# Performance work log

Measured on AMD Instinct MI355X. Metric: run time of the kernel, lower is better.

The kernel has to match this reference:

```python
import jax, jax.numpy as jnp
import numpy as np

B, T, D, H = 32, 512, 512, 8
DH = D // H  # 64


def _pos_enc(t, d):
    # pos / 10000^(2i/d) for ALL i, then sin on even cols, cos on odd cols, scaled by sqrt(d)
    pos = np.arange(t, dtype=np.float64)[:, None]
    i = np.arange(d, dtype=np.float64)[None, :]
    ang = pos / np.power(10000.0, 2.0 * i / d)
    pe = np.empty((t, d), dtype=np.float64)
    pe[:, 0::2] = np.sin(ang[:, 0::2])
    pe[:, 1::2] = np.cos(ang[:, 1::2])
    return jnp.asarray(pe * np.sqrt(float(d)), dtype=jnp.float32)


def setup_inputs() -> dict:
    key = jax.random.key(0)
    ks = jax.random.split(key, 9)
    return {
        "queries": jax.random.normal(ks[0], (B, T, D), dtype=jnp.float32),
        "keys": jax.random.normal(ks[1], (B, T, D), dtype=jnp.float32),
        "query_masks": jax.random.randint(ks[2], (B,), 0, T, dtype=jnp.int32),
        "key_masks": jax.random.randint(ks[3], (B,), 0, T, dtype=jnp.int32),
        "W_Q": jax.random.normal(ks[4], (D, D), dtype=jnp.float32) * 0.05,
        "W_K": jax.random.normal(ks[5], (D, D), dtype=jnp.float32) * 0.05,
        "W_V": jax.random.normal(ks[6], (D, D), dtype=jnp.float32) * 0.05,
        "fw1": jax.random.normal(ks[7], (D, 4 * D), dtype=jnp.float32) * 0.05,
        "fw2": jax.random.normal(ks[8], (4 * D, D), dtype=jnp.float32) * 0.05,
    }


def reference(queries, keys, query_masks, key_masks, W_Q, W_K, W_V, fw1, fw2):
    pe = _pos_enc(T, D)  # [T, D]
    # Source bug kept: queries = posenc(queries); keys = posenc(queries)  -> keys input unused
    q1 = queries + pe[None]          # [B,T,D]
    k1 = q1 + pe[None]               # pos-encoded twice
    Q = q1 @ W_Q                     # [B,T,D]
    Kp = k1 @ W_K                    # [B,T,D]
    V = Kp @ W_V                     # source bug kept: values from projected keys
    # split heads (head-major fold in the original concat(split) idiom)
    Qh = Q.reshape(B, T, H, DH).transpose(2, 0, 1, 3)   # [H,B,T,dh]
    Kh = Kp.reshape(B, T, H, DH).transpose(2, 0, 1, 3)
    Vh = V.reshape(B, T, H, DH).transpose(2, 0, 1, 3)
    scores = jnp.einsum('hbqd,hbkd->hbqk', Qh, Kh) / jnp.sqrt(jnp.float32(DH))
    # source subtracts max over the QUERY axis (axis=1 of [H*B,T,T]) = axis 2 here
    scores = scores - scores.max(axis=2, keepdims=True)
    attn = jax.nn.softmax(scores, axis=-1)
    qmask = (jnp.arange(T)[None, :] < query_masks[:, None]).astype(jnp.float32)  # [B,T]
    attn = attn * qmask[None, :, :, None]
    out = jnp.einsum('hbqk,hbkd->hbqd', attn, Vh)       # [H,B,T,dh]
    result = out.transpose(1, 2, 0, 3).reshape(B, T, D) + q1  # residual with pos-encoded queries
    hidden = jax.nn.relu(result @ fw1)                  # [B,T,4D]
    result = result + hidden @ fw2                      # residual; no layer norm (use_layer_norm=False)
    return result
```

## Files before the change

kernel.cpp:

```cpp
#include <hip/hip_runtime.h>
#include <cstdint>
#include <cstddef>

typedef __bf16 bf16x8 __attribute__((ext_vector_type(8)));
typedef float f32x4 __attribute__((ext_vector_type(4)));
using u16 = unsigned short;
using u32 = unsigned int;

__device__ __forceinline__ u16 f2b(float f) {
  u32 u = __float_as_uint(f);
  u32 r = u + 0x7FFFu + ((u >> 16) & 1u);
  return (u16)(r >> 16);
}
__device__ __forceinline__ float b2f(u16 h) { return __uint_as_float((u32)h << 16); }

__device__ __forceinline__ void gload16(const void* g, void* l) {
  __builtin_amdgcn_global_load_lds((const __attribute__((address_space(1))) void*)g,
                                   (__attribute__((address_space(3))) void*)l, 16, 0, 0);
}

__device__ __forceinline__ u32 mapf(float f) {
  u32 u = __float_as_uint(f);
  return (u & 0x80000000u) ? ~u : (u | 0x80000000u);
}
__device__ __forceinline__ float unmapf(u32 k) {
  u32 u = (k & 0x80000000u) ? (k ^ 0x80000000u) : ~k;
  return __uint_as_float(u);
}
__device__ __forceinline__ u32 cvtpk(float lo, float hi) {
  u32 r;
  asm("v_cvt_pk_bf16_f32 %0, %1, %2" : "=v"(r) : "v"(lo), "v"(hi));
  return r;
}

#define MFMA __builtin_amdgcn_mfma_f32_16x16x32_bf16

__global__ void pe_kernel(float* __restrict__ pe) {
  int i = blockIdx.x * 256 + threadIdx.x;
  if (i >= 512 * 512) return;
  int t = i >> 9, d = i & 511;
  double ang = (double)t * exp((double)d * (-2.0 / 512.0) * log(10000.0));
  double v = (d & 1) ? cos(ang) : sin(ang);
  pe[i] = (float)(v * 22.627416997969522);
}

__global__ void wconv_kernel(const float* __restrict__ WQ, const float* __restrict__ WK,
                             const float* __restrict__ WV, const float* __restrict__ f1,
                             const float* __restrict__ f2,
                             u16* __restrict__ WQth, u16* __restrict__ WQtl,
                             u16* __restrict__ WKth, u16* __restrict__ WKtl,
                             u16* __restrict__ WKb, u16* __restrict__ WVt,
                             u16* __restrict__ f1t, u16* __restrict__ f2t) {
  int i = blockIdx.x * 256 + threadIdx.x;
  if (i < 262144) {
    int n = i >> 9, k = i & 511;
    float wq = WQ[k * 512 + n];
    u16 h = f2b(wq);
    WQth[i] = h;
    WQtl[i] = f2b(wq - b2f(h));
    float wk = WK[k * 512 + n];
    h = f2b(wk);
    WKth[i] = h;
    WKtl[i] = f2b(wk - b2f(h));
    WKb[i] = f2b(WK[i]);
    WVt[i] = f2b(WV[k * 512 + n]);
  } else if (i < 262144 + 1048576) {
    int i2 = i - 262144;
    int n = i2 >> 9, k = i2 & 511;
    f1t[i2] = f2b(f1[k * 2048 + n]);
  } else if (i < 262144 + 2097152) {
    int i3 = i - 262144 - 1048576;
    int n = i3 >> 11, k = i3 & 2047;
    f2t[i3] = f2b(f2[k * 512 + n]);
  }
}

__global__ void prep_kernel(const float* __restrict__ q, const float* __restrict__ pe,
                            u16* __restrict__ q1h, u16* __restrict__ q1l,
                            u16* __restrict__ k1h, u16* __restrict__ k1l,
                            u32* __restrict__ m0) {
  int i = blockIdx.x * 256 + threadIdx.x;
  if (i < 131072) m0[i] = 0u;
  if (i >= 32 * 512 * 512) return;
  int td = i & (262144 - 1);
  float p = pe[td];
  float q1 = q[i] + p;
  float k1 = q1 + p;
  u16 h = f2b(q1);
  q1h[i] = h;
  q1l[i] = f2b(q1 - b2f(h));
  h = f2b(k1);
  k1h[i] = h;
  k1l[i] = f2b(k1 - b2f(h));
}

#define GM_BF16 0
#define GM_RELU 2
#define GM_ADDF32 3

template <int MODE>
__global__ __launch_bounds__(256, 3) void gemm_bt(const u16* __restrict__ A,
                                                  const u16* __restrict__ B, int M, int N, int K,
                                                  u16* __restrict__ outb, float* __restrict__ outf,
                                                  const float* __restrict__ res) {
  __shared__ u16 As[128 * 32];
  __shared__ u16 Bs[128 * 32];
  const int tid = threadIdx.x, lane = tid & 63, w = tid >> 6;
  const int wm = w >> 1, wn = w & 1;
  const long aBase = (long)blockIdx.x * 128;
  const long bBase = (long)blockIdx.y * 128;
  f32x4 acc[4][4] = {};
  const int nk = K >> 5;
  for (int kt = 0; kt < nk; ++kt) {
#pragma unroll
    for (int i = 0; i < 2; ++i) {
      const int c = w * 2 + i;
      const int off = c * 1024 + lane * 16;
      const int r = off >> 6, cb = off & 63;
      gload16((const char*)A + ((aBase + r) * (long)K + (long)kt * 32) * 2 + cb,
              (char*)As + c * 1024);
      gload16((const char*)B + ((bBase + r) * (long)K + (long)kt * 32) * 2 + cb,
              (char*)Bs + c * 1024);
    }
    __syncthreads();
    bf16x8 af[4], bfr[4];
#pragma unroll
    for (int x = 0; x < 4; ++x) {
      af[x] = *(const bf16x8*)&As[(wm * 64 + x * 16 + (lane & 15)) * 32 + (lane >> 4) * 8];
      bfr[x] = *(const bf16x8*)&Bs[(wn * 64 + x * 16 + (lane & 15)) * 32 + (lane >> 4) * 8];
    }
#pragma unroll
    for (int mf = 0; mf < 4; ++mf)
#pragma unroll
      for (int nf = 0; nf < 4; ++nf)
        acc[mf][nf] = MFMA(af[mf], bfr[nf], acc[mf][nf], 0, 0, 0);
    __syncthreads();
  }
#pragma unroll
  for (int mf = 0; mf < 4; ++mf)
#pragma unroll
    for (int nf = 0; nf < 4; ++nf) {
      const long row0 = aBase + wm * 64 + mf * 16 + (lane >> 4) * 4;
      const long col = bBase + wn * 64 + nf * 16 + (lane & 15);
#pragma unroll
      for (int j = 0; j < 4; ++j) {
        float v = acc[mf][nf][j];
        const long row = row0 + j;
        if constexpr (MODE == GM_BF16)
          outb[row * N + col] = f2b(v);
        else if constexpr (MODE == GM_RELU)
          outb[row * N + col] = f2b(v > 0.f ? v : 0.f);
        else
          outf[row * N + col] = res[row * N + col] + v;
      }
    }
}

__global__ __launch_bounds__(256, 2) void gemm_split(const u16* __restrict__ Ah,
                                                     const u16* __restrict__ Al,
                                                     const u16* __restrict__ Bh,
                                                     const u16* __restrict__ Bl, int M, int N,
                                                     int K, u16* __restrict__ Oh,
                                                     u16* __restrict__ Ol) {
  __shared__ u16 Ash[4096], Asl[4096], Bsh[4096], Bsl[4096];
  const int tid = threadIdx.x, lane = tid & 63, w = tid >> 6;
  const int wm = w >> 1, wn = w & 1;
  const long aBase = (long)blockIdx.x * 128;
  const long bBase = (long)blockIdx.y * 128;
  f32x4 acc[4][4] = {};
  const int nk = K >> 5;
  for (int kt = 0; kt < nk; ++kt) {
#pragma unroll
    for (int i = 0; i < 2; ++i) {
      const int c = w * 2 + i;
      const int off = c * 1024 + lane * 16;
      const int r = off >> 6, cb = off & 63;
      long ga = ((aBase + r) * (long)K + (long)kt * 32) * 2 + cb;
      long gb = ((bBase + r) * (long)K + (long)kt * 32) * 2 + cb;
      gload16((const char*)Ah + ga, (char*)Ash + c * 1024);
      gload16((const char*)Al + ga, (char*)Asl + c * 1024);
      gload16((const char*)Bh + gb, (char*)Bsh + c * 1024);
      gload16((const char*)Bl + gb, (char*)Bsl + c * 1024);
    }
    __syncthreads();
    bf16x8 ah[4], al[4], bh[4], bl[4];
#pragma unroll
    for (int x = 0; x < 4; ++x) {
      int ao = (wm * 64 + x * 16 + (lane & 15)) * 32 + (lane >> 4) * 8;
      int bo = (wn * 64 + x * 16 + (lane & 15)) * 32 + (lane >> 4) * 8;
      ah[x] = *(const bf16x8*)&Ash[ao];
      al[x] = *(const bf16x8*)&Asl[ao];
      bh[x] = *(const bf16x8*)&Bsh[bo];
      bl[x] = *(const bf16x8*)&Bsl[bo];
    }
#pragma unroll
    for (int mf = 0; mf < 4; ++mf)
#pragma unroll
      for (int nf = 0; nf < 4; ++nf) {
        acc[mf][nf] = MFMA(ah[mf], bh[nf], acc[mf][nf], 0, 0, 0);
        acc[mf][nf] = MFMA(ah[mf], bl[nf], acc[mf][nf], 0, 0, 0);
        acc[mf][nf] = MFMA(al[mf], bh[nf], acc[mf][nf], 0, 0, 0);
      }
    __syncthreads();
  }
#pragma unroll
  for (int mf = 0; mf < 4; ++mf)
#pragma unroll
    for (int nf = 0; nf < 4; ++nf) {
      const long row0 = aBase + wm * 64 + mf * 16 + (lane >> 4) * 4;
      const long col = bBase + wn * 64 + nf * 16 + (lane & 15);
#pragma unroll
      for (int j = 0; j < 4; ++j) {
        float v = acc[mf][nf][j];
        const long row = row0 + j;
        u16 h = f2b(v);
        Oh[row * N + col] = h;
        Ol[row * N + col] = f2b(v - b2f(h));
      }
    }
}

__global__ __launch_bounds__(256, 4) void attn_colmax(const u16* __restrict__ Qh,
                                                      const u16* __restrict__ Ql,
                                                      const u16* __restrict__ Kh,
                                                      const u16* __restrict__ Kl,
                                                      u32* __restrict__ mg) {
  __shared__ u16 Qsh[4096], Qsl[4096];
  __shared__ u16 Ksh[4096], Ksl[4096];
  __shared__ u32 mloc[512];
  const int tid = threadIdx.x, lane = tid & 63, w = tid >> 6;
  const int ql = lane & 15, g = lane >> 4;
  const int hb = blockIdx.x, b = hb >> 3, h = hb & 7, qc = blockIdx.y;
  mloc[tid] = 0u;
  mloc[tid + 256] = 0u;
  const int srccb = 16 * ((lane & 7) ^ ((lane >> 3) & 7));
#pragma unroll
  for (int i = 0; i < 2; ++i) {
    const int c = w * 2 + i;
    const int r = c * 8 + (lane >> 3);
    long gb = ((long)(b * 512 + qc * 64 + r) * 512 + h * 64) * 2 + srccb;
    gload16((const char*)Qh + gb, (char*)Qsh + c * 1024);
    gload16((const char*)Ql + gb, (char*)Qsl + c * 1024);
  }
  __syncthreads();
  const int qrow = w * 16 + ql;
  const int sw0 = ((g * 16) ^ ((ql & 7) * 16)) >> 1;
  const int sw1 = ((64 + g * 16) ^ ((ql & 7) * 16)) >> 1;
  bf16x8 qh0 = *(const bf16x8*)&Qsh[qrow * 64 + sw0];
  bf16x8 ql0 = *(const bf16x8*)&Qsl[qrow * 64 + sw0];
  bf16x8 qh1 = *(const bf16x8*)&Qsh[qrow * 64 + sw1];
  bf16x8 ql1 = *(const bf16x8*)&Qsl[qrow * 64 + sw1];
  for (int kc = 0; kc < 8; ++kc) {
#pragma unroll
    for (int i = 0; i < 2; ++i) {
      const int c = w * 2 + i;
      const int r = c * 8 + (lane >> 3);
      long gb = ((long)(b * 512 + kc * 64 + r) * 512 + h * 64) * 2 + srccb;
      gload16((const char*)Kh + gb, (char*)Ksh + c * 1024);
      gload16((const char*)Kl + gb, (char*)Ksl + c * 1024);
    }
    __syncthreads();
#pragma unroll
    for (int kt = 0; kt < 4; ++kt) {
      const int krow = kt * 16 + ql;
      bf16x8 kh0 = *(const bf16x8*)&Ksh[krow * 64 + sw0];
      bf16x8 kl0 = *(const bf16x8*)&Ksl[krow * 64 + sw0];
      bf16x8 kh1 = *(const bf16x8*)&Ksh[krow * 64 + sw1];
      bf16x8 kl1 = *(const bf16x8*)&Ksl[krow * 64 + sw1];
      f32x4 acc = {0.f, 0.f, 0.f, 0.f};
      acc = MFMA(qh0, kh0, acc, 0, 0, 0);
      acc = MFMA(qh0, kl0, acc, 0, 0, 0);
      acc = MFMA(ql0, kh0, acc, 0, 0, 0);
      acc = MFMA(qh1, kh1, acc, 0, 0, 0);
      acc = MFMA(qh1, kl1, acc, 0, 0, 0);
      acc = MFMA(ql1, kh1, acc, 0, 0, 0);
      float v = fmaxf(fmaxf(acc[0], acc[1]), fmaxf(acc[2], acc[3]));
      v = fmaxf(v, __shfl_xor(v, 16));
      v = fmaxf(v, __shfl_xor(v, 32));
      if (lane < 16) atomicMax(&mloc[kc * 64 + kt * 16 + ql], mapf(v));
    }
    __syncthreads();
  }
  for (int k = tid; k < 512; k += 256) atomicMax(&mg[(long)hb * 512 + k], mloc[k]);
}

__global__ __launch_bounds__(256, 3) void attn_main(
    const u16* __restrict__ Qh, const u16* __restrict__ Ql, const u16* __restrict__ Kh,
    const u16* __restrict__ Kl, const u16* __restrict__ Vt, const u32* __restrict__ mg,
    const int* __restrict__ qmask, const u16* __restrict__ q1h, const u16* __restrict__ q1l,
    float* __restrict__ resf, u16* __restrict__ resb) {
  __shared__ u16 Qsh[4096], Qsl[4096];
  __shared__ u16 Ksh[4096], Ksl[4096];
  __shared__ float mks[512];
  const int tid = threadIdx.x, lane = tid & 63, w = tid >> 6;
  const int qll = lane & 15, g = lane >> 4;
  const int hb = blockIdx.x, b = hb >> 3, h = hb & 7, qc = blockIdx.y;
  const int qm = qmask[b];
  for (int k = tid; k < 512; k += 256) mks[k] = 0.125f * unmapf(mg[(long)hb * 512 + k]);
  const int srccb = 16 * ((lane & 7) ^ ((lane >> 3) & 7));
#pragma unroll
  for (int i = 0; i < 2; ++i) {
    const int c = w * 2 + i;
    const int r = c * 8 + (lane >> 3);
    long gb = ((long)(b * 512 + qc * 64 + r) * 512 + h * 64) * 2 + srccb;
    gload16((const char*)Qh + gb, (char*)Qsh + c * 1024);
    gload16((const char*)Ql + gb, (char*)Qsl + c * 1024);
  }
  __syncthreads();
  const int qrow = w * 16 + qll;
  const int sw0 = ((g * 16) ^ ((qll & 7) * 16)) >> 1;
  const int sw1 = ((64 + g * 16) ^ ((qll & 7) * 16)) >> 1;
  bf16x8 qh0 = *(const bf16x8*)&Qsh[qrow * 64 + sw0];
  bf16x8 qh1 = *(const bf16x8*)&Qsh[qrow * 64 + sw1];
  bf16x8 qlo0 = *(const bf16x8*)&Qsl[qrow * 64 + sw0];
  bf16x8 qlo1 = *(const bf16x8*)&Qsl[qrow * 64 + sw1];
  f32x4 o[4] = {};
  float mr = -3.0e38f, rsum = 0.f;
  const u16* vb = Vt + (long)(h * 64) * 16384 + b * 512;
  const int src0 = (g & 1) * 32 + qll;
  const int src1 = src0 + 16;
  const bool lowh = g < 2;
  for (int kc = 0; kc < 8; ++kc) {
    bf16x8 vf[2][4];
#pragma unroll
    for (int k2 = 0; k2 < 2; ++k2)
#pragma unroll
      for (int nf = 0; nf < 4; ++nf)
        vf[k2][nf] =
            *(const bf16x8*)&vb[(long)(nf * 16 + qll) * 16384 + (kc * 2 + k2) * 32 + g * 8];
#pragma unroll
    for (int i = 0; i < 2; ++i) {
      const int c = w * 2 + i;
      const int r = c * 8 + (lane >> 3);
      long gb = ((long)(b * 512 + kc * 64 + r) * 512 + h * 64) * 2 + srccb;
      gload16((const char*)Kh + gb, (char*)Ksh + c * 1024);
      gload16((const char*)Kl + gb, (char*)Ksl + c * 1024);
    }
    __syncthreads();
    f32x4 s4[4] = {};
#pragma unroll
    for (int kt = 0; kt < 4; ++kt) {
      const int krow = kt * 16 + qll;
      bf16x8 kh0 = *(const bf16x8*)&Ksh[krow * 64 + sw0];
      bf16x8 kl0 = *(const bf16x8*)&Ksl[krow * 64 + sw0];
      bf16x8 kh1 = *(const bf16x8*)&Ksh[krow * 64 + sw1];
      bf16x8 kl1 = *(const bf16x8*)&Ksl[krow * 64 + sw1];
      s4[kt] = MFMA(kh0, qh0, s4[kt], 0, 0, 0);
      s4[kt] = MFMA(kh0, qlo0, s4[kt], 0, 0, 0);
      s4[kt] = MFMA(kl0, qh0, s4[kt], 0, 0, 0);
      s4[kt] = MFMA(kh1, qh1, s4[kt], 0, 0, 0);
      s4[kt] = MFMA(kh1, qlo1, s4[kt], 0, 0, 0);
      s4[kt] = MFMA(kl1, qh1, s4[kt], 0, 0, 0);
    }
    __syncthreads();
    float pm = mr;
#pragma unroll
    for (int kt = 0; kt < 4; ++kt) {
      f32x4 mrow = *(const f32x4*)&mks[kc * 64 + kt * 16 + g * 4];
#pragma unroll
      for (int j = 0; j < 4; ++j) {
        float z = s4[kt][j] * 0.125f - mrow[j];
        s4[kt][j] = z;
        pm = fmaxf(pm, z);
      }
    }
    pm = fmaxf(pm, __shfl_xor(pm, 16));
    pm = fmaxf(pm, __shfl_xor(pm, 32));
    const float f = __expf(mr - pm);
    mr = pm;
    rsum *= f;
#pragma unroll
    for (int nf = 0; nf < 4; ++nf) {
      o[nf][0] *= f;
      o[nf][1] *= f;
      o[nf][2] *= f;
      o[nf][3] *= f;
    }
    u32 pk0[4], pk1[4];
#pragma unroll
    for (int kt = 0; kt < 4; ++kt) {
      float p0 = __expf(s4[kt][0] - mr);
      float p1 = __expf(s4[kt][1] - mr);
      float p2 = __expf(s4[kt][2] - mr);
      float p3 = __expf(s4[kt][3] - mr);
      rsum += (p0 + p1) + (p2 + p3);
      pk0[kt] = cvtpk(p0, p1);
      pk1[kt] = cvtpk(p2, p3);
    }
#pragma unroll
    for (int k2 = 0; k2 < 2; ++k2) {
      const int fA = 2 * k2, fB = 2 * k2 + 1;
      u32 a00 = __shfl(pk0[fA], src0), b00 = __shfl(pk0[fB], src0);
      u32 a10 = __shfl(pk1[fA], src0), b10 = __shfl(pk1[fB], src0);
      u32 a01 = __shfl(pk0[fA], src1), b01 = __shfl(pk0[fB], src1);
      u32 a11 = __shfl(pk1[fA], src1), b11 = __shfl(pk1[fB], src1);
      union {
        u32 u[4];
        bf16x8 v;
      } pf;
      pf.u[0] = lowh ? a00 : b00;
      pf.u[1] = lowh ? a10 : b10;
      pf.u[2] = lowh ? a01 : b01;
      pf.u[3] = lowh ? a11 : b11;
#pragma unroll
      for (int nf = 0; nf < 4; ++nf) o[nf] = MFMA(vf[k2][nf], pf.v, o[nf], 0, 0, 0);
    }
  }
  rsum += __shfl_xor(rsum, 16);
  rsum += __shfl_xor(rsum, 32);
  const int qg = qc * 64 + w * 16 + qll;
  const float sc = (qg < qm) ? (1.0f / rsum) : 0.0f;
#pragma unroll
  for (int nf = 0; nf < 4; ++nf) {
    const int col = h * 64 + nf * 16 + g * 4;
    const long idx = (long)(b * 512 + qg) * 512 + col;
    ushort4 qh4 = *(const ushort4*)&q1h[idx];
    ushort4 ql4 = *(const ushort4*)&q1l[idx];
    float v0 = o[nf][0] * sc + b2f(qh4.x) + b2f(ql4.x);
    float v1 = o[nf][1] * sc + b2f(qh4.y) + b2f(ql4.y);
    float v2 = o[nf][2] * sc + b2f(qh4.z) + b2f(ql4.z);
    float v3 = o[nf][3] * sc + b2f(qh4.w) + b2f(ql4.w);
    *(float4*)&resf[idx] = make_float4(v0, v1, v2, v3);
    ushort4 rb = {f2b(v0), f2b(v1), f2b(v2), f2b(v3)};
    *(ushort4*)&resb[idx] = rb;
  }
}

extern "C" void kernel_launch(void* const* d_in, const int* in_sizes, int n_in, void* d_out,
                              int out_size, void* d_ws, size_t ws_size, hipStream_t stream) {
  (void)in_sizes;
  (void)n_in;
  (void)out_size;
  (void)ws_size;
  const float* queries = (const float*)d_in[0];
  const int* qmask = (const int*)d_in[2];
  const float* WQ = (const float*)d_in[4];
  const float* WK = (const float*)d_in[5];
  const float* WV = (const float*)d_in[6];
  const float* f1 = (const float*)d_in[7];
  const float* f2 = (const float*)d_in[8];
  float* out = (float*)d_out;
  char* ws = (char*)d_ws;
  const size_t A = 16777216;
  u16* q1h = (u16*)(ws + 0 * A);
  u16* q1l = (u16*)(ws + 1 * A);
  u16* k1h = (u16*)(ws + 2 * A);
  u16* k1l = (u16*)(ws + 3 * A);
  u16* Qh = (u16*)(ws + 4 * A);
  u16* Ql = (u16*)(ws + 5 * A);
  u16* Kh = (u16*)(ws + 6 * A);
  u16* Kl = (u16*)(ws + 7 * A);
  u16* Vt = (u16*)(ws + 8 * A);
  u16* resb = (u16*)(ws + 9 * A);
  u16* hid = (u16*)(ws + 2 * A);
  hid = (u16*)(ws + 0 * A);
  float* pe = (float*)(ws + 10 * A);
  u32* m_ws = (u32*)(ws + 10 * A + 1048576);
  char* wbase = ws + 10 * A + 1572864;
  u16* WQth = (u16*)(wbase + 0 * 524288);
  u16* WQtl = (u16*)(wbase + 1 * 524288);
  u16* WKth = (u16*)(wbase + 2 * 524288);
  u16* WKtl = (u16*)(wbase + 3 * 524288);
  u16* WKb = (u16*)(wbase + 4 * 524288);
  u16* WVt_w = (u16*)(wbase + 5 * 524288);
  u16* WKVt = (u16*)(wbase + 6 * 524288);
  u16* f1t = (u16*)(wbase + 7 * 524288);
  u16* f2t = (u16*)(wbase + 7 * 524288 + 2097152);

  pe_kernel<<<1024, 256, 0, stream>>>(pe);
  wconv_kernel<<<9216, 256, 0, stream>>>(WQ, WK, WV, f1, f2, WQth, WQtl, WKth, WKtl, WKb, WVt_w,
                                         f1t, f2t);
  prep_kernel<<<32768, 256, 0, stream>>>(queries, pe, q1h, q1l, k1h, k1l, m_ws);
  gemm_bt<GM_BF16><<<dim3(4, 4), 256, 0, stream>>>(WVt_w, WKb, 512, 512, 512, WKVt, nullptr,
                                                   nullptr);
  gemm_split<<<dim3(128, 4), 256, 0, stream>>>(q1h, q1l, WQth, WQtl, 16384, 512, 512, Qh, Ql);
  gemm_split<<<dim3(128, 4), 256, 0, stream>>>(k1h, k1l, WKth, WKtl, 16384, 512, 512, Kh, Kl);
  gemm_bt<GM_BF16><<<dim3(4, 128), 256, 0, stream>>>(WKVt, k1h, 512, 16384, 512, Vt, nullptr,
                                                     nullptr);
  attn_colmax<<<dim3(256, 8), 256, 0, stream>>>(Qh, Ql, Kh, Kl, m_ws);
  attn_main<<<dim3(256, 8), 256, 0, stream>>>(Qh, Ql, Kh, Kl, Vt, m_ws, qmask, q1h, q1l, out,
                                              resb);
  gemm_bt<GM_RELU><<<dim3(128, 16), 256, 0, stream>>>(resb, f1t, 16384, 2048, 512, hid, nullptr,
                                                      nullptr);
  gemm_bt<GM_ADDF32><<<dim3(128, 4), 256, 0, stream>>>(hid, f2t, 16384, 512, 2048, nullptr, out,
                                                       out);
}
```

Baseline: 365.0 us.

## Load Q/K fragments directly from global memory in attention kernels, dropping LDS staging

Both attention kernels (the column-max pass and the main pass) now read Q and K MFMA fragments straight from global memory into registers instead of staging them through swizzled shared memory, which removes the LDS buffers and most of the block barriers. The column-max kernel also drops its shared-memory max reduction and issues atomicMax directly to global memory. This cuts LDS use and synchronization, which may raise occupancy, but K tiles are now fetched redundantly by each of the four waves through cache and there are many more global atomics.

```diff
diff --git a/kernel.cpp b/kernel.cpp
--- a/kernel.cpp
+++ b/kernel.cpp
@@ -225,48 +225,23 @@
                                                       const u16* __restrict__ Kh,
                                                       const u16* __restrict__ Kl,
                                                       u32* __restrict__ mg) {
-  __shared__ u16 Qsh[4096], Qsl[4096];
-  __shared__ u16 Ksh[4096], Ksl[4096];
-  __shared__ u32 mloc[512];
   const int tid = threadIdx.x, lane = tid & 63, w = tid >> 6;
-  const int ql = lane & 15, g = lane >> 4;
+  const int qll = lane & 15, g = lane >> 4;
   const int hb = blockIdx.x, b = hb >> 3, h = hb & 7, qc = blockIdx.y;
-  mloc[tid] = 0u;
-  mloc[tid + 256] = 0u;
-  const int srccb = 16 * ((lane & 7) ^ ((lane >> 3) & 7));
-#pragma unroll
-  for (int i = 0; i < 2; ++i) {
-    const int c = w * 2 + i;
-    const int r = c * 8 + (lane >> 3);
-    long gb = ((long)(b * 512 + qc * 64 + r) * 512 + h * 64) * 2 + srccb;
-    gload16((const char*)Qh + gb, (char*)Qsh + c * 1024);
-    gload16((const char*)Ql + gb, (char*)Qsl + c * 1024);
-  }
-  __syncthreads();
-  const int qrow = w * 16 + ql;
-  const int sw0 = ((g * 16) ^ ((ql & 7) * 16)) >> 1;
-  const int sw1 = ((64 + g * 16) ^ ((ql & 7) * 16)) >> 1;
-  bf16x8 qh0 = *(const bf16x8*)&Qsh[qrow * 64 + sw0];
-  bf16x8 ql0 = *(const bf16x8*)&Qsl[qrow * 64 + sw0];
-  bf16x8 qh1 = *(const bf16x8*)&Qsh[qrow * 64 + sw1];
-  bf16x8 ql1 = *(const bf16x8*)&Qsl[qrow * 64 + sw1];
+  const long qrow = (long)(b * 512 + qc * 64 + w * 16 + qll) * 512 + h * 64 + g * 8;
+  bf16x8 qh0 = *(const bf16x8*)&Qh[qrow];
+  bf16x8 qh1 = *(const bf16x8*)&Qh[qrow + 32];
+  bf16x8 ql0 = *(const bf16x8*)&Ql[qrow];
+  bf16x8 ql1 = *(const bf16x8*)&Ql[qrow + 32];
+  u32* mghb = mg + (long)hb * 512;
   for (int kc = 0; kc < 8; ++kc) {
 #pragma unroll
-    for (int i = 0; i < 2; ++i) {
-      const int c = w * 2 + i;
-      const int r = c * 8 + (lane >> 3);
-      long gb = ((long)(b * 512 + kc * 64 + r) * 512 + h * 64) * 2 + srccb;
-      gload16((const char*)Kh + gb, (char*)Ksh + c * 1024);
-      gload16((const char*)Kl + gb, (char*)Ksl + c * 1024);
-    }
-    __syncthreads();
-#pragma unroll
     for (int kt = 0; kt < 4; ++kt) {
-      const int krow = kt * 16 + ql;
-      bf16x8 kh0 = *(const bf16x8*)&Ksh[krow * 64 + sw0];
-      bf16x8 kl0 = *(const bf16x8*)&Ksl[krow * 64 + sw0];
-      bf16x8 kh1 = *(const bf16x8*)&Ksh[krow * 64 + sw1];
-      bf16x8 kl1 = *(const bf16x8*)&Ksl[krow * 64 + sw1];
+      const long kr = (long)(b * 512 + kc * 64 + kt * 16 + qll) * 512 + h * 64 + g * 8;
+      bf16x8 kh0 = *(const bf16x8*)&Kh[kr];
+      bf16x8 kh1 = *(const bf16x8*)&Kh[kr + 32];
+      bf16x8 kl0 = *(const bf16x8*)&Kl[kr];
+      bf16x8 kl1 = *(const bf16x8*)&Kl[kr + 32];
       f32x4 acc = {0.f, 0.f, 0.f, 0.f};
       acc = MFMA(qh0, kh0, acc, 0, 0, 0);
       acc = MFMA(qh0, kl0, acc, 0, 0, 0);
@@ -277,11 +252,9 @@
       float v = fmaxf(fmaxf(acc[0], acc[1]), fmaxf(acc[2], acc[3]));
       v = fmaxf(v, __shfl_xor(v, 16));
       v = fmaxf(v, __shfl_xor(v, 32));
-      if (lane < 16) atomicMax(&mloc[kc * 64 + kt * 16 + ql], mapf(v));
-    }
-    __syncthreads();
-  }
-  for (int k = tid; k < 512; k += 256) atomicMax(&mg[(long)hb * 512 + k], mloc[k]);
+      if (lane < 16) atomicMax(&mghb[kc * 64 + kt * 16 + qll], mapf(v));
+    }
+  }
 }
 
 __global__ __launch_bounds__(256, 3) void attn_main(
@@ -289,31 +262,18 @@
     const u16* __restrict__ Kl, const u16* __restrict__ Vt, const u32* __restrict__ mg,
     const int* __restrict__ qmask, const u16* __restrict__ q1h, const u16* __restrict__ q1l,
     float* __restrict__ resf, u16* __restrict__ resb) {
-  __shared__ u16 Qsh[4096], Qsl[4096];
-  __shared__ u16 Ksh[4096], Ksl[4096];
   __shared__ float mks[512];
   const int tid = threadIdx.x, lane = tid & 63, w = tid >> 6;
   const int qll = lane & 15, g = lane >> 4;
   const int hb = blockIdx.x, b = hb >> 3, h = hb & 7, qc = blockIdx.y;
   const int qm = qmask[b];
   for (int k = tid; k < 512; k += 256) mks[k] = 0.125f * unmapf(mg[(long)hb * 512 + k]);
-  const int srccb = 16 * ((lane & 7) ^ ((lane >> 3) & 7));
-#pragma unroll
-  for (int i = 0; i < 2; ++i) {
-    const int c = w * 2 + i;
-    const int r = c * 8 + (lane >> 3);
-    long gb = ((long)(b * 512 + qc * 64 + r) * 512 + h * 64) * 2 + srccb;
-    gload16((const char*)Qh + gb, (char*)Qsh + c * 1024);
-    gload16((const char*)Ql + gb, (char*)Qsl + c * 1024);
-  }
   __syncthreads();
-  const int qrow = w * 16 + qll;
-  const int sw0 = ((g * 16) ^ ((qll & 7) * 16)) >> 1;
-  const int sw1 = ((64 + g * 16) ^ ((qll & 7) * 16)) >> 1;
-  bf16x8 qh0 = *(const bf16x8*)&Qsh[qrow * 64 + sw0];
-  bf16x8 qh1 = *(const bf16x8*)&Qsh[qrow * 64 + sw1];
-  bf16x8 qlo0 = *(const bf16x8*)&Qsl[qrow * 64 + sw0];
-  bf16x8 qlo1 = *(const bf16x8*)&Qsl[qrow * 64 + sw1];
+  const long qrow = (long)(b * 512 + qc * 64 + w * 16 + qll) * 512 + h * 64 + g * 8;
+  bf16x8 qh0 = *(const bf16x8*)&Qh[qrow];
+  bf16x8 qh1 = *(const bf16x8*)&Qh[qrow + 32];
+  bf16x8 qlo0 = *(const bf16x8*)&Ql[qrow];
+  bf16x8 qlo1 = *(const bf16x8*)&Ql[qrow + 32];
   f32x4 o[4] = {};
   float mr = -3.0e38f, rsum = 0.f;
   const u16* vb = Vt + (long)(h * 64) * 16384 + b * 512;
@@ -328,23 +288,14 @@
       for (int nf = 0; nf < 4; ++nf)
         vf[k2][nf] =
             *(const bf16x8*)&vb[(long)(nf * 16 + qll) * 16384 + (kc * 2 + k2) * 32 + g * 8];
-#pragma unroll
-    for (int i = 0; i < 2; ++i) {
-      const int c = w * 2 + i;
-      const int r = c * 8 + (lane >> 3);
-      long gb = ((long)(b * 512 + kc * 64 + r) * 512 + h * 64) * 2 + srccb;
-      gload16((const char*)Kh + gb, (char*)Ksh + c * 1024);
-      gload16((const char*)Kl + gb, (char*)Ksl + c * 1024);
-    }
-    __syncthreads();
     f32x4 s4[4] = {};
 #pragma unroll
     for (int kt = 0; kt < 4; ++kt) {
-      const int krow = kt * 16 + qll;
-      bf16x8 kh0 = *(const bf16x8*)&Ksh[krow * 64 + sw0];
-      bf16x8 kl0 = *(const bf16x8*)&Ksl[krow * 64 + sw0];
-      bf16x8 kh1 = *(const bf16x8*)&Ksh[krow * 64 + sw1];
-      bf16x8 kl1 = *(const bf16x8*)&Ksl[krow * 64 + sw1];
+      const long kr = (long)(b * 512 + kc * 64 + kt * 16 + qll) * 512 + h * 64 + g * 8;
+      bf16x8 kh0 = *(const bf16x8*)&Kh[kr];
+      bf16x8 kh1 = *(const bf16x8*)&Kh[kr + 32];
+      bf16x8 kl0 = *(const bf16x8*)&Kl[kr];
+      bf16x8 kl1 = *(const bf16x8*)&Kl[kr + 32];
       s4[kt] = MFMA(kh0, qh0, s4[kt], 0, 0, 0);
       s4[kt] = MFMA(kh0, qlo0, s4[kt], 0, 0, 0);
       s4[kt] = MFMA(kl0, qh0, s4[kt], 0, 0, 0);
@@ -352,7 +303,6 @@
       s4[kt] = MFMA(kh1, qlo1, s4[kt], 0, 0, 0);
       s4[kt] = MFMA(kl1, qh1, s4[kt], 0, 0, 0);
     }
-    __syncthreads();
     float pm = mr;
 #pragma unroll
     for (int kt = 0; kt < 4; ++kt) {
@@ -452,8 +402,7 @@
   u16* Kl = (u16*)(ws + 7 * A);
   u16* Vt = (u16*)(ws + 8 * A);
   u16* resb = (u16*)(ws + 9 * A);
-  u16* hid = (u16*)(ws + 2 * A);
-  hid = (u16*)(ws + 0 * A);
+  u16* hid = (u16*)(ws + 0 * A);
   float* pe = (float*)(ws + 10 * A);
   u32* m_ws = (u32*)(ws + 10 * A + 1048576);
   char* wbase = ws + 10 * A + 1572864;
```

After: 539.6 us. +47.8%, slower.

## Share one LDS buffer for Q and K tiles, raise occupancy, add setprio around MFMA

Applied to the files above, without the earlier changes.

Both attention kernels now stage Q and then K through a single pair of LDS buffers instead of separate ones, which halves shared-memory use and lets launch bounds rise to 6 blocks per CU. The colmax kernel drops its LDS-local max array and does atomicMax directly to global memory. s_setprio is raised around the MFMA sections to favour the matrix work. The risks are more global atomic traffic, an extra barrier, and possible register pressure at the higher occupancy target.

```diff
diff --git a/kernel.cpp b/kernel.cpp
--- a/kernel.cpp
+++ b/kernel.cpp
@@ -220,53 +220,52 @@
     }
 }
 
-__global__ __launch_bounds__(256, 4) void attn_colmax(const u16* __restrict__ Qh,
+__global__ __launch_bounds__(256, 6) void attn_colmax(const u16* __restrict__ Qh,
                                                       const u16* __restrict__ Ql,
                                                       const u16* __restrict__ Kh,
                                                       const u16* __restrict__ Kl,
                                                       u32* __restrict__ mg) {
-  __shared__ u16 Qsh[4096], Qsl[4096];
-  __shared__ u16 Ksh[4096], Ksl[4096];
-  __shared__ u32 mloc[512];
+  __shared__ u16 Bh_s[4096], Bl_s[4096];
   const int tid = threadIdx.x, lane = tid & 63, w = tid >> 6;
-  const int ql = lane & 15, g = lane >> 4;
+  const int qll = lane & 15, g = lane >> 4;
   const int hb = blockIdx.x, b = hb >> 3, h = hb & 7, qc = blockIdx.y;
-  mloc[tid] = 0u;
-  mloc[tid + 256] = 0u;
   const int srccb = 16 * ((lane & 7) ^ ((lane >> 3) & 7));
 #pragma unroll
   for (int i = 0; i < 2; ++i) {
     const int c = w * 2 + i;
     const int r = c * 8 + (lane >> 3);
     long gb = ((long)(b * 512 + qc * 64 + r) * 512 + h * 64) * 2 + srccb;
-    gload16((const char*)Qh + gb, (char*)Qsh + c * 1024);
-    gload16((const char*)Ql + gb, (char*)Qsl + c * 1024);
+    gload16((const char*)Qh + gb, (char*)Bh_s + c * 1024);
+    gload16((const char*)Ql + gb, (char*)Bl_s + c * 1024);
   }
   __syncthreads();
-  const int qrow = w * 16 + ql;
-  const int sw0 = ((g * 16) ^ ((ql & 7) * 16)) >> 1;
-  const int sw1 = ((64 + g * 16) ^ ((ql & 7) * 16)) >> 1;
-  bf16x8 qh0 = *(const bf16x8*)&Qsh[qrow * 64 + sw0];
-  bf16x8 ql0 = *(const bf16x8*)&Qsl[qrow * 64 + sw0];
-  bf16x8 qh1 = *(const bf16x8*)&Qsh[qrow * 64 + sw1];
-  bf16x8 ql1 = *(const bf16x8*)&Qsl[qrow * 64 + sw1];
+  const int qrow = w * 16 + qll;
+  const int sw0 = ((g * 16) ^ ((qll & 7) * 16)) >> 1;
+  const int sw1 = ((64 + g * 16) ^ ((qll & 7) * 16)) >> 1;
+  bf16x8 qh0 = *(const bf16x8*)&Bh_s[qrow * 64 + sw0];
+  bf16x8 ql0 = *(const bf16x8*)&Bl_s[qrow * 64 + sw0];
+  bf16x8 qh1 = *(const bf16x8*)&Bh_s[qrow * 64 + sw1];
+  bf16x8 ql1 = *(const bf16x8*)&Bl_s[qrow * 64 + sw1];
+  __syncthreads();
+  u32* mghb = mg + (long)hb * 512;
   for (int kc = 0; kc < 8; ++kc) {
 #pragma unroll
     for (int i = 0; i < 2; ++i) {
       const int c = w * 2 + i;
       const int r = c * 8 + (lane >> 3);
       long gb = ((long)(b * 512 + kc * 64 + r) * 512 + h * 64) * 2 + srccb;
-      gload16((const char*)Kh + gb, (char*)Ksh + c * 1024);
-      gload16((const char*)Kl + gb, (char*)Ksl + c * 1024);
-    }
-    __syncthreads();
+      gload16((const char*)Kh + gb, (char*)Bh_s + c * 1024);
+      gload16((const char*)Kl + gb, (char*)Bl_s + c * 1024);
+    }
+    __syncthreads();
+    __builtin_amdgcn_s_setprio(1);
 #pragma unroll
     for (int kt = 0; kt < 4; ++kt) {
-      const int krow = kt * 16 + ql;
-      bf16x8 kh0 = *(const bf16x8*)&Ksh[krow * 64 + sw0];
-      bf16x8 kl0 = *(const bf16x8*)&Ksl[krow * 64 + sw0];
-      bf16x8 kh1 = *(const bf16x8*)&Ksh[krow * 64 + sw1];
-      bf16x8 kl1 = *(const bf16x8*)&Ksl[krow * 64 + sw1];
+      const int krow = kt * 16 + qll;
+      bf16x8 kh0 = *(const bf16x8*)&Bh_s[krow * 64 + sw0];
+      bf16x8 kl0 = *(const bf16x8*)&Bl_s[krow * 64 + sw0];
+      bf16x8 kh1 = *(const bf16x8*)&Bh_s[krow * 64 + sw1];
+      bf16x8 kl1 = *(const bf16x8*)&Bl_s[krow * 64 + sw1];
       f32x4 acc = {0.f, 0.f, 0.f, 0.f};
       acc = MFMA(qh0, kh0, acc, 0, 0, 0);
       acc = MFMA(qh0, kl0, acc, 0, 0, 0);
@@ -277,43 +276,43 @@
       float v = fmaxf(fmaxf(acc[0], acc[1]), fmaxf(acc[2], acc[3]));
       v = fmaxf(v, __shfl_xor(v, 16));
       v = fmaxf(v, __shfl_xor(v, 32));
-      if (lane < 16) atomicMax(&mloc[kc * 64 + kt * 16 + ql], mapf(v));
-    }
-    __syncthreads();
-  }
-  for (int k = tid; k < 512; k += 256) atomicMax(&mg[(long)hb * 512 + k], mloc[k]);
-}
-
-__global__ __launch_bounds__(256, 3) void attn_main(
+      if (lane < 16) atomicMax(&mghb[kc * 64 + kt * 16 + qll], mapf(v));
+    }
+    __builtin_amdgcn_s_setprio(0);
+    __syncthreads();
+  }
+}
+
+__global__ __launch_bounds__(256, 6) void attn_main(
     const u16* __restrict__ Qh, const u16* __restrict__ Ql, const u16* __restrict__ Kh,
     const u16* __restrict__ Kl, const u16* __restrict__ Vt, const u32* __restrict__ mg,
     const int* __restrict__ qmask, const u16* __restrict__ q1h, const u16* __restrict__ q1l,
     float* __restrict__ resf, u16* __restrict__ resb) {
-  __shared__ u16 Qsh[4096], Qsl[4096];
-  __shared__ u16 Ksh[4096], Ksl[4096];
+  __shared__ u16 Bh_s[4096], Bl_s[4096];
   __shared__ float mks[512];
   const int tid = threadIdx.x, lane = tid & 63, w = tid >> 6;
   const int qll = lane & 15, g = lane >> 4;
   const int hb = blockIdx.x, b = hb >> 3, h = hb & 7, qc = blockIdx.y;
   const int qm = qmask[b];
-  for (int k = tid; k < 512; k += 256) mks[k] = 0.125f * unmapf(mg[(long)hb * 512 + k]);
   const int srccb = 16 * ((lane & 7) ^ ((lane >> 3) & 7));
 #pragma unroll
   for (int i = 0; i < 2; ++i) {
     const int c = w * 2 + i;
     const int r = c * 8 + (lane >> 3);
     long gb = ((long)(b * 512 + qc * 64 + r) * 512 + h * 64) * 2 + srccb;
-    gload16((const char*)Qh + gb, (char*)Qsh + c * 1024);
-    gload16((const char*)Ql + gb, (char*)Qsl + c * 1024);
-  }
+    gload16((const char*)Qh + gb, (char*)Bh_s + c * 1024);
+    gload16((const char*)Ql + gb, (char*)Bl_s + c * 1024);
+  }
+  for (int k = tid; k < 512; k += 256) mks[k] = 0.125f * unmapf(mg[(long)hb * 512 + k]);
   __syncthreads();
   const int qrow = w * 16 + qll;
   const int sw0 = ((g * 16) ^ ((qll & 7) * 16)) >> 1;
   const int sw1 = ((64 + g * 16) ^ ((qll & 7) * 16)) >> 1;
-  bf16x8 qh0 = *(const bf16x8*)&Qsh[qrow * 64 + sw0];
-  bf16x8 qh1 = *(const bf16x8*)&Qsh[qrow * 64 + sw1];
-  bf16x8 qlo0 = *(const bf16x8*)&Qsl[qrow * 64 + sw0];
-  bf16x8 qlo1 = *(const bf16x8*)&Qsl[qrow * 64 + sw1];
+  bf16x8 qh0 = *(const bf16x8*)&Bh_s[qrow * 64 + sw0];
+  bf16x8 qh1 = *(const bf16x8*)&Bh_s[qrow * 64 + sw1];
+  bf16x8 qlo0 = *(const bf16x8*)&Bl_s[qrow * 64 + sw0];
+  bf16x8 qlo1 = *(const bf16x8*)&Bl_s[qrow * 64 + sw1];
+  __syncthreads();
   f32x4 o[4] = {};
   float mr = -3.0e38f, rsum = 0.f;
   const u16* vb = Vt + (long)(h * 64) * 16384 + b * 512;
@@ -333,18 +332,19 @@
       const int c = w * 2 + i;
       const int r = c * 8 + (lane >> 3);
       long gb = ((long)(b * 512 + kc * 64 + r) * 512 + h * 64) * 2 + srccb;
-      gload16((const char*)Kh + gb, (char*)Ksh + c * 1024);
-      gload16((const char*)Kl + gb, (char*)Ksl + c * 1024);
+      gload16((const char*)Kh + gb, (char*)Bh_s + c * 1024);
+      gload16((const char*)Kl + gb, (char*)Bl_s + c * 1024);
     }
     __syncthreads();
     f32x4 s4[4] = {};
+    __builtin_amdgcn_s_setprio(1);
 #pragma unroll
     for (int kt = 0; kt < 4; ++kt) {
       const int krow = kt * 16 + qll;
-      bf16x8 kh0 = *(const bf16x8*)&Ksh[krow * 64 + sw0];
-      bf16x8 kl0 = *(const bf16x8*)&Ksl[krow * 64 + sw0];
-      bf16x8 kh1 = *(const bf16x8*)&Ksh[krow * 64 + sw1];
-      bf16x8 kl1 = *(const bf16x8*)&Ksl[krow * 64 + sw1];
+      bf16x8 kh0 = *(const bf16x8*)&Bh_s[krow * 64 + sw0];
+      bf16x8 kl0 = *(const bf16x8*)&Bl_s[krow * 64 + sw0];
+      bf16x8 kh1 = *(const bf16x8*)&Bh_s[krow * 64 + sw1];
+      bf16x8 kl1 = *(const bf16x8*)&Bl_s[krow * 64 + sw1];
       s4[kt] = MFMA(kh0, qh0, s4[kt], 0, 0, 0);
       s4[kt] = MFMA(kh0, qlo0, s4[kt], 0, 0, 0);
       s4[kt] = MFMA(kl0, qh0, s4[kt], 0, 0, 0);
@@ -352,6 +352,7 @@
       s4[kt] = MFMA(kh1, qlo1, s4[kt], 0, 0, 0);
       s4[kt] = MFMA(kl1, qh1, s4[kt], 0, 0, 0);
     }
+    __builtin_amdgcn_s_setprio(0);
     __syncthreads();
     float pm = mr;
 #pragma unroll
@@ -387,6 +388,7 @@
       pk0[kt] = cvtpk(p0, p1);
       pk1[kt] = cvtpk(p2, p3);
     }
+    __builtin_amdgcn_s_setprio(1);
 #pragma unroll
     for (int k2 = 0; k2 < 2; ++k2) {
       const int fA = 2 * k2, fB = 2 * k2 + 1;
@@ -405,6 +407,7 @@
 #pragma unroll
       for (int nf = 0; nf < 4; ++nf) o[nf] = MFMA(vf[k2][nf], pf.v, o[nf], 0, 0, 0);
     }
+    __builtin_amdgcn_s_setprio(0);
   }
   rsum += __shfl_xor(rsum, 16);
   rsum += __shfl_xor(rsum, 32);
@@ -452,8 +455,7 @@
   u16* Kl = (u16*)(ws + 7 * A);
   u16* Vt = (u16*)(ws + 8 * A);
   u16* resb = (u16*)(ws + 9 * A);
-  u16* hid = (u16*)(ws + 2 * A);
-  hid = (u16*)(ws + 0 * A);
+  u16* hid = (u16*)(ws + 0 * A);
   float* pe = (float*)(ws + 10 * A);
   u32* m_ws = (u32*)(ws + 10 * A + 1048576);
   char* wbase = ws + 10 * A + 1572864;
```

Result: slower. 511.9 us (+40.2%).
